# Kernel tuning notes

Measured on AMD Instinct MI355X. Metric: run time of the kernel, lower is better.

The kernel has to match this reference:

```python
import jax, jax.numpy as jnp
import numpy as np

B, S, H, NH, HD = 2, 2048, 2048, 16, 128
MASK_VALUE = -1e10


def setup_inputs() -> dict:
    key = jax.random.key(0)
    ks = jax.random.split(key, 5)
    scale = 1.0 / np.sqrt(H)
    x = jax.random.normal(ks[0], (B, S, H), dtype=jnp.float32)
    Wq = jax.random.normal(ks[1], (H, NH * HD), dtype=jnp.float32) * scale
    Wk = jax.random.normal(ks[2], (H, NH * HD), dtype=jnp.float32) * scale
    Wv = jax.random.normal(ks[3], (H, NH * HD), dtype=jnp.float32) * scale
    Wo = jax.random.normal(ks[4], (NH * HD, H), dtype=jnp.float32) * scale
    # causal boolean mask (B, S, S) as in decoder-style gemma usage
    mask = jnp.broadcast_to(jnp.tril(jnp.ones((S, S), dtype=bool)), (B, S, S))
    return {"x": x, "mask": mask, "Wq": Wq, "Wk": Wk, "Wv": Wv, "Wo": Wo}


def reference(x, mask, Wq, Wk, Wv, Wo):
    b, s, h = x.shape
    # bias-free QKV projections, split into heads -> (b, nh, s, hd)
    def split_heads(y):
        return y.reshape(b, s, NH, HD).transpose(0, 2, 1, 3)
    q = split_heads(x @ Wq)
    k = split_heads(x @ Wk)
    v = split_heads(x @ Wv)
    scores = jnp.einsum('bhtd,bhTd->bhtT', q, k) / jnp.sqrt(jnp.asarray(HD, x.dtype))
    scores = jnp.where(mask[:, None, :, :], scores, MASK_VALUE)
    weights = jax.nn.softmax(scores, axis=-1)
    out = jnp.einsum('bhtT,bhTd->bhtd', weights, v)
    out = out.transpose(0, 2, 1, 3).reshape(b, s, NH * HD)
    return out @ Wo
```

## Files before the change

### kernel.cpp

```cpp
#include <hip/hip_runtime.h>
#include <hip/hip_bf16.h>
#include <stdint.h>

#define DEVFN __device__ __forceinline__

typedef __attribute__((ext_vector_type(8))) short short8;
typedef __attribute__((ext_vector_type(4))) float f32x4;
typedef __attribute__((ext_vector_type(16))) float f32x16;

constexpr int S_LEN = 2048;
constexpr int HDIM  = 2048;
constexpr int NHEAD = 16;
constexpr int HD    = 128;

DEVFN unsigned short f2bf(float f){
  union { float f; unsigned u; } x; x.f = f;
  unsigned r = x.u + 0x7fffu + ((x.u >> 16) & 1u);
  return (unsigned short)(r >> 16);
}

typedef const __attribute__((address_space(1))) void* gas1_ptr;
typedef __attribute__((address_space(3))) void* las3_ptr;

DEVFN void gl_lds16(const void* g, void* l){
  __builtin_amdgcn_global_load_lds((gas1_ptr)g, (las3_ptr)l, 16, 0, 0);
}

DEVFN f32x4 mfma16(short8 a, short8 b, f32x4 c){
  return __builtin_amdgcn_mfma_f32_16x16x32_bf16(a, b, c, 0, 0, 0);
}

DEVFN f32x16 mfma32(short8 a, short8 b, f32x16 c){
  return __builtin_amdgcn_mfma_f32_32x32x16_bf16(a, b, c, 0, 0, 0);
}

DEVFN unsigned cvtpk_bf16(float lo, float hi){
  unsigned w;
  asm("v_cvt_pk_bf16_f32 %0, %1, %2" : "=v"(w) : "v"(lo), "v"(hi));
  return w;
}


__global__ void cast_x_kernel(const float* __restrict__ in, unsigned short* __restrict__ out){
  int i = (blockIdx.x * 256 + threadIdx.x) * 4;
  float4 v = *(const float4*)(in + i);
  ushort4 o;
  o.x = f2bf(v.x); o.y = f2bf(v.y); o.z = f2bf(v.z); o.w = f2bf(v.w);
  *(ushort4*)(out + i) = o;
}

__global__ void transpose_cast_w4(const float* __restrict__ w0, const float* __restrict__ w1,
                                  const float* __restrict__ w2, const float* __restrict__ w3,
                                  unsigned short* __restrict__ out){
  __shared__ float tile[32][33];
  int tx = threadIdx.x, ty = threadIdx.y;
  int kb = blockIdx.x * 32, nb = blockIdx.y * 32, z = blockIdx.z;
  const float* in = (z == 0) ? w0 : (z == 1) ? w1 : (z == 2) ? w2 : w3;
  unsigned short* op = out + (size_t)z * HDIM * HDIM;
  #pragma unroll
  for (int i = 0; i < 4; i++)
    tile[ty + i*8][tx] = in[(size_t)(kb + ty + i*8) * HDIM + nb + tx];
  __syncthreads();
  #pragma unroll
  for (int i = 0; i < 4; i++)
    op[(size_t)(nb + ty + i*8) * HDIM + kb + tx] = f2bf(tile[tx][ty + i*8]);
}


DEVFN void gemm_core_bt(const unsigned short* __restrict__ A,
                        const unsigned short* __restrict__ Bt,
                        int K, int m0, int n0, char* ls, f32x4 (&acc)[4][4]){
  const int t = threadIdx.x;
  const int wid = t >> 6, lane = t & 63;
  const int wr = wid >> 1, wc = wid & 1;
  const int l15 = lane & 15, lg = lane >> 4;
  char* lsA = ls;
  char* lsB = ls + 16384;

  for (int k0 = 0; k0 < K; k0 += 64){
    __syncthreads();
    #pragma unroll
    for (int i = 0; i < 4; i++){
      int o = (t + i*256) * 16;
      int row = o >> 7;
      int col = (o & 127) ^ ((row & 7) << 4);
      gl_lds16((const char*)A + ((size_t)(m0 + row) * K + k0) * 2 + col, lsA + o);
    }
    #pragma unroll
    for (int i = 0; i < 4; i++){
      int o = (t + i*256) * 16;
      int row = o >> 7;
      int col = (o & 127) ^ ((row & 7) << 4);
      gl_lds16((const char*)Bt + ((size_t)(n0 + row) * K + k0) * 2 + col, lsB + o);
    }
    __syncthreads();
    #pragma unroll
    for (int kk = 0; kk < 2; kk++){
      short8 af[4], bfr[4];
      #pragma unroll
      for (int i = 0; i < 4; i++){
        int ra = wr*64 + i*16 + l15;
        af[i]  = *(const short8*)(lsA + ra*128 + ((kk*64 + lg*16) ^ ((ra & 7) << 4)));
        int rb = wc*64 + i*16 + l15;
        bfr[i] = *(const short8*)(lsB + rb*128 + ((kk*64 + lg*16) ^ ((rb & 7) << 4)));
      }
      #pragma unroll
      for (int i = 0; i < 4; i++)
        #pragma unroll
        for (int j = 0; j < 4; j++)
          acc[i][j] = mfma16(af[i], bfr[j], acc[i][j]);
    }
  }
}

__global__ __launch_bounds__(256, 4)
void gemm_qkv(const unsigned short* __restrict__ xb, const unsigned short* __restrict__ Wt,
              unsigned short* __restrict__ Qb, unsigned short* __restrict__ Kb,
              unsigned short* __restrict__ Vt){
  __shared__ __align__(16) char ls[32768];
  f32x4 acc[4][4];
  const f32x4 z4 = {0.f, 0.f, 0.f, 0.f};
  #pragma unroll
  for (int i = 0; i < 4; i++)
    #pragma unroll
    for (int j = 0; j < 4; j++) acc[i][j] = z4;

  const int m0 = blockIdx.x * 128;
  const int n0 = blockIdx.y * 128;
  gemm_core_bt(xb, Wt, HDIM, m0, n0, ls, acc);

  const float qscale = 0.08838834764831845f * 1.4426950408889634f;
  const int t = threadIdx.x, wid = t >> 6, lane = t & 63;
  const int wr = wid >> 1, wc = wid & 1, l15 = lane & 15, lg = lane >> 4;
  const int bb = m0 >> 11, ss0 = m0 & 2047;

  if (n0 < 4096){
    unsigned short* base = (n0 < 2048) ? Qb : Kb;
    const float sc = (n0 < 2048) ? qscale : 1.0f;
    #pragma unroll
    for (int j = 0; j < 4; j++){
      int n = n0 + wc*64 + j*16 + l15;
      int hh = (n >> 7) & 15, d = n & 127;
      #pragma unroll
      for (int i = 0; i < 4; i++){
        #pragma unroll
        for (int r = 0; r < 4; r++){
          int ss = ss0 + wr*64 + i*16 + lg*4 + r;
          base[(((size_t)bb * NHEAD + hh) * S_LEN + ss) * HD + d] = f2bf(acc[i][j][r] * sc);
        }
      }
    }
  } else {
    const int hh = (n0 - 4096) >> 7;
    __syncthreads();
    #pragma unroll
    for (int j = 0; j < 4; j++){
      int nn = wc*64 + j*16 + l15;
      int rowb = nn*256 + (((nn & 7) << 4));
      #pragma unroll
      for (int i = 0; i < 4; i++){
        int mmb = (wr*64 + i*16 + lg*4) * 2;
        unsigned w0 = cvtpk_bf16(acc[i][j][0], acc[i][j][1]);
        unsigned w1 = cvtpk_bf16(acc[i][j][2], acc[i][j][3]);
        *(unsigned*)(ls + nn*256 + ((mmb    ) ^ ((nn & 7) << 4))) = w0;
        *(unsigned*)(ls + nn*256 + ((mmb + 4) ^ ((nn & 7) << 4))) = w1;
      }
      (void)rowb;
    }
    __syncthreads();
    unsigned short* vout = Vt + (((size_t)bb * NHEAD + hh) * HD) * S_LEN;
    #pragma unroll
    for (int p = 0; p < 8; p++){
      int idx = p*256 + t;
      int d = idx >> 4;
      int m8 = (idx & 15) * 8;
      short8 v = *(const short8*)(ls + d*256 + ((m8*2) ^ ((d & 7) << 4)));
      *(short8*)(vout + (size_t)d * S_LEN + ss0 + m8) = v;
    }
  }
}

__global__ __launch_bounds__(256, 4)
void gemm_out(const unsigned short* __restrict__ Ob, const unsigned short* __restrict__ Wot,
              float* __restrict__ out){
  __shared__ __align__(16) char ls[32768];
  f32x4 acc[4][4];
  const f32x4 z4 = {0.f, 0.f, 0.f, 0.f};
  #pragma unroll
  for (int i = 0; i < 4; i++)
    #pragma unroll
    for (int j = 0; j < 4; j++) acc[i][j] = z4;

  const int m0 = blockIdx.x * 128;
  const int n0 = blockIdx.y * 128;
  gemm_core_bt(Ob, Wot, HDIM, m0, n0, ls, acc);

  const int t = threadIdx.x, wid = t >> 6, lane = t & 63;
  const int wr = wid >> 1, wc = wid & 1, l15 = lane & 15, lg = lane >> 4;
  #pragma unroll
  for (int i = 0; i < 4; i++){
    #pragma unroll
    for (int r = 0; r < 4; r++){
      int m = m0 + wr*64 + i*16 + lg*4 + r;
      #pragma unroll
      for (int j = 0; j < 4; j++){
        int n = n0 + wc*64 + j*16 + l15;
        out[(size_t)m * HDIM + n] = acc[i][j][r];
      }
    }
  }
}

__global__ __launch_bounds__(256, 2)
void attn_kernel(const unsigned short* __restrict__ Q,
                 const unsigned short* __restrict__ Kg,
                 const unsigned short* __restrict__ Vt,
                 unsigned short* __restrict__ Ob){
  __shared__ __align__(16) unsigned short Kl[2][64*128];
  __shared__ __align__(16) unsigned short Vl[2][128*64];

  const int t = threadIdx.x;
  const int wid = t >> 6, lane = t & 63;
  const int l31 = lane & 31, hi = lane >> 5;
  const int L = blockIdx.x;
  const int bh = L & 31;
  const int z = L >> 5;
  const int qt = (z < 8) ? z : 23 - z;
  const int b = bh >> 4, h = bh & 15;
  const unsigned short* Qp = Q  + (size_t)bh * S_LEN * HD;
  const unsigned short* Kp = Kg + (size_t)bh * S_LEN * HD;
  const unsigned short* Vp = Vt + (size_t)bh * S_LEN * HD;
  const int q0 = qt * 128;
  const int wrow0 = q0 + wid * 32;
  const int qrow = wrow0 + l31;
  const int nt = 2 * qt + 2;

  auto stage = [&](int buf, int k0){
    #pragma unroll
    for (int i = 0; i < 4; i++){
      int o = (t + i*256) * 16;
      int row = o >> 8;
      int col = (o & 255) ^ ((row & 15) << 4);
      gl_lds16((const char*)(Kp + (size_t)(k0 + row) * HD) + col, (char*)&Kl[buf][0] + o);
    }
    #pragma unroll
    for (int i = 0; i < 4; i++){
      int o = (t + i*256) * 16;
      int row = o >> 7;
      int col = (o & 127) ^ ((row & 7) << 4);
      gl_lds16((const char*)(Vp + (size_t)row * S_LEN + k0) + col, (char*)&Vl[buf][0] + o);
    }
  };

  short8 qf[8];
  #pragma unroll
  for (int dk = 0; dk < 8; dk++)
    qf[dk] = *(const short8*)(Qp + (size_t)qrow * HD + dk*16 + hi*8);

  f32x16 oacc[4];
  #pragma unroll
  for (int db = 0; db < 4; db++)
    #pragma unroll
    for (int r = 0; r < 16; r++) oacc[db][r] = 0.f;
  float mrun = -1e30f, lsum = 0.f;

  stage(0, 0);
  asm volatile("s_waitcnt vmcnt(0)" ::: "memory");
  __builtin_amdgcn_s_barrier();

  int cur = 0;
  #pragma unroll 1
  for (int tdx = 0; tdx < nt; tdx++){
    if (tdx + 1 < nt) stage(cur ^ 1, (tdx + 1) * 64);
    const int k0 = tdx * 64;

    if (k0 <= wrow0 + 31){
      const char* Kb_ = (const char*)&Kl[cur][0];
      const char* Vb_ = (const char*)&Vl[cur][0];

      f32x16 sacc[2];
      #pragma unroll
      for (int cb = 0; cb < 2; cb++)
        #pragma unroll
        for (int r = 0; r < 16; r++) sacc[cb][r] = 0.f;
      __builtin_amdgcn_s_setprio(1);
      #pragma unroll
      for (int dk = 0; dk < 8; dk++){
        #pragma unroll
        for (int cb = 0; cb < 2; cb++){
          int kr = cb*32 + l31;
          short8 af = *(const short8*)(Kb_ + kr*256 + ((dk*32 + hi*16) ^ ((kr & 15) << 4)));
          sacc[cb] = mfma32(af, qf[dk], sacc[cb]);
        }
      }
      __builtin_amdgcn_s_setprio(0);

      if (k0 + 64 > wrow0){
        #pragma unroll
        for (int cb = 0; cb < 2; cb++)
          #pragma unroll
          for (int r = 0; r < 16; r++){
            int kcol = k0 + cb*32 + (r & 3) + 8*(r >> 2) + 4*hi;
            if (kcol > qrow) sacc[cb][r] = -1e30f;
          }
      }

      float mv[8];
      #pragma unroll
      for (int i = 0; i < 8; i++)
        mv[i] = fmaxf(fmaxf(sacc[0][i], sacc[0][i+8]), fmaxf(sacc[1][i], sacc[1][i+8]));
      #pragma unroll
      for (int s = 4; s > 0; s >>= 1)
        #pragma unroll
        for (int i = 0; i < 4; i++)
          if (i < s) mv[i] = fmaxf(mv[i], mv[i+s]);
      float mx = fmaxf(mv[0], __shfl_xor(mv[0], 32, 64));
      if (!__all(mx <= mrun + 8.f)){
        float mnew = fmaxf(mrun, mx);
        float alpha = exp2f(mrun - mnew);
        mrun = mnew;
        lsum *= alpha;
        #pragma unroll
        for (int db = 0; db < 4; db++)
          #pragma unroll
          for (int r = 0; r < 16; r++) oacc[db][r] *= alpha;
      }
      float ls = 0.f;
      #pragma unroll
      for (int cb = 0; cb < 2; cb++)
        #pragma unroll
        for (int r = 0; r < 16; r++){
          float p = exp2f(sacc[cb][r] - mrun);
          sacc[cb][r] = p;
          ls += p;
        }
      lsum += ls;

      short8 pa[4];
      #pragma unroll
      for (int ks = 0; ks < 4; ks++){
        int cb = ks >> 1, bs = (ks & 1) * 8;
        unsigned A1 = cvtpk_bf16(sacc[cb][bs+4], sacc[cb][bs+5]);
        unsigned B1 = cvtpk_bf16(sacc[cb][bs+0], sacc[cb][bs+1]);
        unsigned A2 = cvtpk_bf16(sacc[cb][bs+6], sacc[cb][bs+7]);
        unsigned B2 = cvtpk_bf16(sacc[cb][bs+2], sacc[cb][bs+3]);
        unsigned oA1 = __shfl_xor(A1, 32, 64), oB1 = __shfl_xor(B1, 32, 64);
        unsigned oA2 = __shfl_xor(A2, 32, 64), oB2 = __shfl_xor(B2, 32, 64);
        union { unsigned u[4]; short8 v; } pk;
        pk.u[0] = hi ? oA1 : B1;
        pk.u[1] = hi ? oA2 : B2;
        pk.u[2] = hi ? A1 : oB1;
        pk.u[3] = hi ? A2 : oB2;
        pa[ks] = pk.v;
      }

      __builtin_amdgcn_s_setprio(1);
      #pragma unroll
      for (int ks = 0; ks < 4; ks++){
        #pragma unroll
        for (int db = 0; db < 4; db++){
          int vr = db*32 + l31;
          short8 vf = *(const short8*)(Vb_ + vr*128 + ((ks*32 + hi*16) ^ ((vr & 7) << 4)));
          oacc[db] = mfma32(vf, pa[ks], oacc[db]);
        }
      }
      __builtin_amdgcn_s_setprio(0);
    }

    asm volatile("s_waitcnt vmcnt(0)" ::: "memory");
    __builtin_amdgcn_s_barrier();
    cur ^= 1;
  }

  float lt = lsum + __shfl_xor(lsum, 32, 64);
  float inv = 1.f / lt;
  #pragma unroll
  for (int db = 0; db < 4; db++)
    #pragma unroll
    for (int r = 0; r < 16; r++) oacc[db][r] *= inv;

  char* reg_lds = (char*)&Kl[0][0] + wid * 8192;
  #pragma unroll
  for (int ms = 0; ms < 8; ms++){
    int db = ms >> 1, bs = (ms & 1) * 8;
    unsigned A1 = cvtpk_bf16(oacc[db][bs+4], oacc[db][bs+5]);
    unsigned B1 = cvtpk_bf16(oacc[db][bs+0], oacc[db][bs+1]);
    unsigned A2 = cvtpk_bf16(oacc[db][bs+6], oacc[db][bs+7]);
    unsigned B2 = cvtpk_bf16(oacc[db][bs+2], oacc[db][bs+3]);
    unsigned oA1 = __shfl_xor(A1, 32, 64), oB1 = __shfl_xor(B1, 32, 64);
    unsigned oA2 = __shfl_xor(A2, 32, 64), oB2 = __shfl_xor(B2, 32, 64);
    union { unsigned u[4]; short8 v; } pk;
    pk.u[0] = hi ? oA1 : B1;
    pk.u[1] = hi ? oA2 : B2;
    pk.u[2] = hi ? A1 : oB1;
    pk.u[3] = hi ? A2 : oB2;
    int byteo = l31*256 + ((ms*32 + hi*16) ^ ((l31 & 7) << 4));
    *(short8*)(reg_lds + byteo) = pk.v;
  }
  #pragma unroll
  for (int i = 0; i < 8; i++){
    int r = (lane >> 4) + i*4;
    int c = lane & 15;
    short8 v = *(const short8*)(reg_lds + r*256 + ((c*16) ^ ((r & 7) << 4)));
    *(short8*)(Ob + ((size_t)(b * S_LEN + wrow0 + r)) * 2048 + h*128 + c*8) = v;
  }
}

extern "C" void kernel_launch(void* const* d_in, const int* in_sizes, int n_in,
                              void* d_out, int out_size, void* d_ws, size_t ws_size,
                              hipStream_t stream){
  const float* x  = (const float*)d_in[0];
  const float* Wq = (const float*)d_in[2];
  const float* Wk = (const float*)d_in[3];
  const float* Wv = (const float*)d_in[4];
  const float* Wo = (const float*)d_in[5];

  char* ws = (char*)d_ws;
  unsigned short* xb  = (unsigned short*)(ws);
  unsigned short* Wt  = (unsigned short*)(ws + 16777216);
  unsigned short* Wot = (unsigned short*)(ws + 41943040);
  unsigned short* Qb  = (unsigned short*)(ws + 50331648);
  unsigned short* Kb  = (unsigned short*)(ws + 67108864);
  unsigned short* Vt  = (unsigned short*)(ws + 83886080);
  unsigned short* Ob  = xb;

  dim3 tb(32, 8);
  cast_x_kernel<<<8192, 256, 0, stream>>>(x, xb);
  transpose_cast_w4<<<dim3(64, 64, 4), tb, 0, stream>>>(Wq, Wk, Wv, Wo, Wt);

  gemm_qkv<<<dim3(32, 48), 256, 0, stream>>>(xb, Wt, Qb, Kb, Vt);

  attn_kernel<<<512, 256, 0, stream>>>(Qb, Kb, Vt, Ob);

  gemm_out<<<dim3(32, 16), 256, 0, stream>>>(Ob, Wot, (float*)d_out);
}
```

Baseline: 242.7 us.

## Software-pipeline attention PV with next QK and use permlane32 swaps

Restructures the attention loop so the P·V MFMAs of the previous tile run interleaved with the QK^T MFMAs of the current tile. The V buffer becomes triple-buffered so the delayed P·V can still read it, and the loop is unrolled by two to ping-pong the P fragment registers. Each wave now stops at its own causal limit rather than the block-wide one. The cross-half shuffles used for the bf16 repacks are replaced with v_permlane32_swap. The aim is to hide the softmax latency and cut ds_bpermute traffic, at the cost of more LDS and more live registers.

```diff
diff --git a/kernel.cpp b/kernel.cpp
--- a/kernel.cpp
+++ b/kernel.cpp
@@ -156,7 +156,6 @@
     #pragma unroll
     for (int j = 0; j < 4; j++){
       int nn = wc*64 + j*16 + l15;
-      int rowb = nn*256 + (((nn & 7) << 4));
       #pragma unroll
       for (int i = 0; i < 4; i++){
         int mmb = (wr*64 + i*16 + lg*4) * 2;
@@ -165,7 +164,6 @@
         *(unsigned*)(ls + nn*256 + ((mmb    ) ^ ((nn & 7) << 4))) = w0;
         *(unsigned*)(ls + nn*256 + ((mmb + 4) ^ ((nn & 7) << 4))) = w1;
       }
-      (void)rowb;
     }
     __syncthreads();
     unsigned short* vout = Vt + (((size_t)bb * NHEAD + hh) * HD) * S_LEN;
@@ -217,7 +215,7 @@
                  const unsigned short* __restrict__ Vt,
                  unsigned short* __restrict__ Ob){
   __shared__ __align__(16) unsigned short Kl[2][64*128];
-  __shared__ __align__(16) unsigned short Vl[2][128*64];
+  __shared__ __align__(16) unsigned short Vl[3][128*64];
 
   const int t = threadIdx.x;
   const int wid = t >> 6, lane = t & 63;
@@ -234,21 +232,25 @@
   const int wrow0 = q0 + wid * 32;
   const int qrow = wrow0 + l31;
   const int nt = 2 * qt + 2;
-
-  auto stage = [&](int buf, int k0){
+  const int ntw = (wrow0 >> 6) + 1;
+
+  auto stage = [&](int tdx){
+    char* kb = (char*)&Kl[tdx & 1][0];
+    char* vb = (char*)&Vl[tdx % 3][0];
+    const int k0 = tdx * 64;
     #pragma unroll
     for (int i = 0; i < 4; i++){
       int o = (t + i*256) * 16;
       int row = o >> 8;
       int col = (o & 255) ^ ((row & 15) << 4);
-      gl_lds16((const char*)(Kp + (size_t)(k0 + row) * HD) + col, (char*)&Kl[buf][0] + o);
+      gl_lds16((const char*)(Kp + (size_t)(k0 + row) * HD) + col, kb + o);
     }
     #pragma unroll
     for (int i = 0; i < 4; i++){
       int o = (t + i*256) * 16;
       int row = o >> 7;
       int col = (o & 127) ^ ((row & 7) << 4);
-      gl_lds16((const char*)(Vp + (size_t)row * S_LEN + k0) + col, (char*)&Vl[buf][0] + o);
+      gl_lds16((const char*)(Vp + (size_t)row * S_LEN + k0) + col, vb + o);
     }
   };
 
@@ -263,22 +265,30 @@
     #pragma unroll
     for (int r = 0; r < 16; r++) oacc[db][r] = 0.f;
   float mrun = -1e30f, lsum = 0.f;
-
-  stage(0, 0);
-  asm volatile("s_waitcnt vmcnt(0)" ::: "memory");
-  __builtin_amdgcn_s_barrier();
-
-  int cur = 0;
-  #pragma unroll 1
-  for (int tdx = 0; tdx < nt; tdx++){
-    if (tdx + 1 < nt) stage(cur ^ 1, (tdx + 1) * 64);
-    const int k0 = tdx * 64;
-
-    if (k0 <= wrow0 + 31){
-      const char* Kb_ = (const char*)&Kl[cur][0];
-      const char* Vb_ = (const char*)&Vl[cur][0];
-
-      f32x16 sacc[2];
+  short8 paA[4], paB[4];
+
+  auto do_pv = [&](short8 (&pprev)[4], const char* vb){
+    __builtin_amdgcn_s_setprio(1);
+    #pragma unroll
+    for (int ks = 0; ks < 4; ks++){
+      #pragma unroll
+      for (int db = 0; db < 4; db++){
+        int vr = db*32 + l31;
+        short8 vf = *(const short8*)(vb + vr*128 + ((ks*32 + hi*16) ^ ((vr & 7) << 4)));
+        oacc[db] = mfma32(vf, pprev[ks], oacc[db]);
+      }
+    }
+    __builtin_amdgcn_s_setprio(0);
+  };
+
+  auto body = [&](int tdx, short8 (&pcur)[4], short8 (&pprev)[4]){
+    if (tdx + 1 < nt) stage(tdx + 1);
+    const char* Kb_ = (const char*)&Kl[tdx & 1][0];
+    const bool doQK = (tdx < ntw);
+    const bool doPV = (tdx >= 1) && (tdx <= ntw);
+
+    f32x16 sacc[2];
+    if (doQK){
       #pragma unroll
       for (int cb = 0; cb < 2; cb++)
         #pragma unroll
@@ -294,8 +304,13 @@
         }
       }
       __builtin_amdgcn_s_setprio(0);
-
-      if (k0 + 64 > wrow0){
+    }
+
+    if (doPV) do_pv(pprev, (const char*)&Vl[(tdx - 1) % 3][0]);
+
+    if (doQK){
+      const int k0 = tdx * 64;
+      if (tdx == ntw - 1){
         #pragma unroll
         for (int cb = 0; cb < 2; cb++)
           #pragma unroll
@@ -304,7 +319,6 @@
             if (kcol > qrow) sacc[cb][r] = -1e30f;
           }
       }
-
       float mv[8];
       #pragma unroll
       for (int i = 0; i < 8; i++)
@@ -335,42 +349,35 @@
           ls += p;
         }
       lsum += ls;
-
-      short8 pa[4];
       #pragma unroll
       for (int ks = 0; ks < 4; ks++){
         int cb = ks >> 1, bs = (ks & 1) * 8;
+        unsigned B1 = cvtpk_bf16(sacc[cb][bs+0], sacc[cb][bs+1]);
+        unsigned B2 = cvtpk_bf16(sacc[cb][bs+2], sacc[cb][bs+3]);
         unsigned A1 = cvtpk_bf16(sacc[cb][bs+4], sacc[cb][bs+5]);
-        unsigned B1 = cvtpk_bf16(sacc[cb][bs+0], sacc[cb][bs+1]);
         unsigned A2 = cvtpk_bf16(sacc[cb][bs+6], sacc[cb][bs+7]);
-        unsigned B2 = cvtpk_bf16(sacc[cb][bs+2], sacc[cb][bs+3]);
-        unsigned oA1 = __shfl_xor(A1, 32, 64), oB1 = __shfl_xor(B1, 32, 64);
-        unsigned oA2 = __shfl_xor(A2, 32, 64), oB2 = __shfl_xor(B2, 32, 64);
+        asm("v_permlane32_swap_b32 %0, %1" : "+v"(B1), "+v"(A1));
+        asm("v_permlane32_swap_b32 %0, %1" : "+v"(B2), "+v"(A2));
         union { unsigned u[4]; short8 v; } pk;
-        pk.u[0] = hi ? oA1 : B1;
-        pk.u[1] = hi ? oA2 : B2;
-        pk.u[2] = hi ? A1 : oB1;
-        pk.u[3] = hi ? A2 : oB2;
-        pa[ks] = pk.v;
-      }
-
-      __builtin_amdgcn_s_setprio(1);
-      #pragma unroll
-      for (int ks = 0; ks < 4; ks++){
-        #pragma unroll
-        for (int db = 0; db < 4; db++){
-          int vr = db*32 + l31;
-          short8 vf = *(const short8*)(Vb_ + vr*128 + ((ks*32 + hi*16) ^ ((vr & 7) << 4)));
-          oacc[db] = mfma32(vf, pa[ks], oacc[db]);
-        }
-      }
-      __builtin_amdgcn_s_setprio(0);
+        pk.u[0] = B1; pk.u[1] = B2; pk.u[2] = A1; pk.u[3] = A2;
+        pcur[ks] = pk.v;
+      }
     }
 
     asm volatile("s_waitcnt vmcnt(0)" ::: "memory");
     __builtin_amdgcn_s_barrier();
-    cur ^= 1;
-  }
+  };
+
+  stage(0);
+  asm volatile("s_waitcnt vmcnt(0)" ::: "memory");
+  __builtin_amdgcn_s_barrier();
+
+  #pragma unroll 1
+  for (int tt = 0; tt < nt; tt += 2){
+    body(tt,     paA, paB);
+    body(tt + 1, paB, paA);
+  }
+  if (ntw == nt) do_pv(paB, (const char*)&Vl[(nt - 1) % 3][0]);
 
   float lt = lsum + __shfl_xor(lsum, 32, 64);
   float inv = 1.f / lt;
@@ -379,21 +386,19 @@
     #pragma unroll
     for (int r = 0; r < 16; r++) oacc[db][r] *= inv;
 
+  __builtin_amdgcn_s_barrier();
   char* reg_lds = (char*)&Kl[0][0] + wid * 8192;
   #pragma unroll
   for (int ms = 0; ms < 8; ms++){
     int db = ms >> 1, bs = (ms & 1) * 8;
+    unsigned B1 = cvtpk_bf16(oacc[db][bs+0], oacc[db][bs+1]);
+    unsigned B2 = cvtpk_bf16(oacc[db][bs+2], oacc[db][bs+3]);
     unsigned A1 = cvtpk_bf16(oacc[db][bs+4], oacc[db][bs+5]);
-    unsigned B1 = cvtpk_bf16(oacc[db][bs+0], oacc[db][bs+1]);
     unsigned A2 = cvtpk_bf16(oacc[db][bs+6], oacc[db][bs+7]);
-    unsigned B2 = cvtpk_bf16(oacc[db][bs+2], oacc[db][bs+3]);
-    unsigned oA1 = __shfl_xor(A1, 32, 64), oB1 = __shfl_xor(B1, 32, 64);
-    unsigned oA2 = __shfl_xor(A2, 32, 64), oB2 = __shfl_xor(B2, 32, 64);
+    asm("v_permlane32_swap_b32 %0, %1" : "+v"(B1), "+v"(A1));
+    asm("v_permlane32_swap_b32 %0, %1" : "+v"(B2), "+v"(A2));
     union { unsigned u[4]; short8 v; } pk;
-    pk.u[0] = hi ? oA1 : B1;
-    pk.u[1] = hi ? oA2 : B2;
-    pk.u[2] = hi ? A1 : oB1;
-    pk.u[3] = hi ? A2 : oB2;
+    pk.u[0] = B1; pk.u[1] = B2; pk.u[2] = A1; pk.u[3] = A2;
     int byteo = l31*256 + ((ms*32 + hi*16) ^ ((l31 & 7) << 4));
     *(short8*)(reg_lds + byteo) = pk.v;
   }
```

Measured after the change: 231.8 us. -4.5%, faster.
